# Kernel optimization log

Measured on AMD Instinct MI355X. Metric: run time of the kernel, lower is better.

The kernel has to match this reference:

```python
import jax, jax.numpy as jnp
import numpy as np

B, S, H = 2, 2048, 2048
NH = 16
HD = H // NH  # 128


def setup_inputs() -> dict:
    key = jax.random.key(0)
    ks = jax.random.split(key, 6)
    sc = 0.02
    return {
        "x": jax.random.normal(ks[0], (B, S, H), dtype=jnp.float32),
        "attention_mask": jnp.zeros((B, S), dtype=jnp.float32),
        "Wq": jax.random.normal(ks[1], (H, H), dtype=jnp.float32) * sc,
        "bq": jnp.zeros((H,), dtype=jnp.float32),
        "Wk": jax.random.normal(ks[2], (H, H), dtype=jnp.float32) * sc,
        "bk": jnp.zeros((H,), dtype=jnp.float32),
        "Wv": jax.random.normal(ks[3], (H, H), dtype=jnp.float32) * sc,
        "bv": jnp.zeros((H,), dtype=jnp.float32),
        "Wo": jax.random.normal(ks[4], (H, H), dtype=jnp.float32) * sc,
        "bo": jnp.zeros((H,), dtype=jnp.float32),
    }


def reference(x, attention_mask, Wq, bq, Wk, bk, Wv, bv, Wo, bo):
    b, s, h = x.shape
    q = (x @ Wq + bq).reshape(b, s, NH, HD)
    k = (x @ Wk + bk).reshape(b, s, NH, HD)
    v = (x @ Wv + bv).reshape(b, s, NH, HD)
    scale = 1.0 / jnp.sqrt(jnp.asarray(HD, dtype=x.dtype))
    scores = jnp.einsum('bqhd,bkhd->bhqk', q, k) * scale
    scores = scores + attention_mask[:, None, None, :]
    weights = jax.nn.softmax(scores, axis=-1)
    attn = jnp.einsum('bhqk,bkhd->bqhd', weights, v).reshape(b, s, h)
    return attn @ Wo + bo
```

## Files before the change

kernel.cpp:

```cpp
#include <hip/hip_runtime.h>
#include <hip/hip_bf16.h>
#include <stdint.h>

#define BB   2
#define SS   2048
#define HHH  2048
#define NHH  16
#define HDD  128
#define MTOT 4096

typedef __bf16 bf16x8 __attribute__((ext_vector_type(8)));
typedef float  f32x4  __attribute__((ext_vector_type(4)));

#define MFMA16(a, b, c) __builtin_amdgcn_mfma_f32_16x16x32_bf16((a), (b), (c), 0, 0, 0)

__device__ __forceinline__ unsigned short f2bf(float f) {
    union { float f; unsigned u; } v; v.f = f;
    unsigned r = v.u + 0x7FFFu + ((v.u >> 16) & 1u);
    return (unsigned short)(r >> 16);
}

__device__ __forceinline__ unsigned packbf(float a, float b) {
    union { __bf16 h[2]; unsigned u; } p;
    p.h[0] = (__bf16)a; p.h[1] = (__bf16)b;
    return p.u;
}

__device__ __forceinline__ void gload16(const void* src, void* lds) {
    __builtin_amdgcn_global_load_lds(
        (__attribute__((address_space(1))) void*)src,
        (__attribute__((address_space(3))) void*)lds,
        16, 0, 0);
}

__global__ void cast_f32_bf16(const float* __restrict__ in,
                              unsigned short* __restrict__ out, int n) {
    int i = (blockIdx.x * blockDim.x + threadIdx.x) * 4;
    int stride = gridDim.x * blockDim.x * 4;
    for (; i < n; i += stride) {
        float4 v = *(const float4*)(in + i);
        ushort4 o;
        o.x = f2bf(v.x); o.y = f2bf(v.y); o.z = f2bf(v.z); o.w = f2bf(v.w);
        *(ushort4*)(out + i) = o;
    }
}

__global__ void transpose_cast(const float* __restrict__ in,
                               unsigned short* __restrict__ out) {
    __shared__ float tile[32][33];
    int c0 = blockIdx.x * 32, r0 = blockIdx.y * 32;
    int tx = threadIdx.x, ty = threadIdx.y;
    #pragma unroll
    for (int i = 0; i < 32; i += 8)
        tile[ty + i][tx] = in[(size_t)(r0 + ty + i) * HHH + c0 + tx];
    __syncthreads();
    #pragma unroll
    for (int i = 0; i < 32; i += 8)
        out[(size_t)(c0 + ty + i) * HHH + r0 + tx] = f2bf(tile[tx][ty + i]);
}

template<int MODE>
__global__ __launch_bounds__(256, 2) void gemm_bf16(
    const unsigned short* __restrict__ A,
    const unsigned short* __restrict__ Bt,
    const float* __restrict__ bias,
    void* __restrict__ Cout,
    int M, int N, int K)
{
    __shared__ __align__(16) unsigned char sm[16384];
    const int tid = threadIdx.x;
    const int wv = tid >> 6, ln = tid & 63;
    const int g = ln >> 4, r = ln & 15;
    const int wr = wv >> 1, wc = wv & 1;
    const int m0 = blockIdx.x * 128, n0 = blockIdx.y * 128;

    size_t srcA[2], srcB[2];
    int ldsA[2], ldsB[2];
    #pragma unroll
    for (int i = 0; i < 2; ++i) {
        int ch = wv * 2 + i;
        int o = ch * 1024 + ln * 16;
        int row = o >> 6;
        int gl = ((o >> 4) & 3) ^ ((row >> 1) & 3);
        ldsA[i] = ch * 1024;
        ldsB[i] = 8192 + ch * 1024;
        srcA[i] = (size_t)(m0 + row) * K + gl * 8;
        srcB[i] = (size_t)(n0 + row) * K + gl * 8;
    }

    f32x4 acc[4][4];
    #pragma unroll
    for (int i = 0; i < 4; ++i)
        #pragma unroll
        for (int j = 0; j < 4; ++j)
            acc[i][j] = (f32x4){0.f, 0.f, 0.f, 0.f};

    for (int kt = 0; kt < K; kt += 32) {
        __syncthreads();
        #pragma unroll
        for (int i = 0; i < 2; ++i) {
            gload16(A + srcA[i] + kt, sm + ldsA[i]);
            gload16(Bt + srcB[i] + kt, sm + ldsB[i]);
        }
        __syncthreads();

        bf16x8 af[4], bfr[4];
        #pragma unroll
        for (int t = 0; t < 4; ++t) {
            int rowa = wr * 64 + t * 16 + r;
            int pha = g ^ ((rowa >> 1) & 3);
            af[t] = *(const bf16x8*)(sm + rowa * 64 + pha * 16);
            int rowb = wc * 64 + t * 16 + r;
            int phb = g ^ ((rowb >> 1) & 3);
            bfr[t] = *(const bf16x8*)(sm + 8192 + rowb * 64 + phb * 16);
        }
        #pragma unroll
        for (int mt = 0; mt < 4; ++mt)
            #pragma unroll
            for (int nt = 0; nt < 4; ++nt)
                acc[mt][nt] = MFMA16(af[mt], bfr[nt], acc[mt][nt]);
    }

    #pragma unroll
    for (int mt = 0; mt < 4; ++mt) {
        #pragma unroll
        for (int nt = 0; nt < 4; ++nt) {
            int col = n0 + wc * 64 + nt * 16 + r;
            float bvv = bias[col];
            f32x4 a = acc[mt][nt];
            int mrow = m0 + wr * 64 + mt * 16 + g * 4;
            if (MODE == 0) {
                #pragma unroll
                for (int q = 0; q < 4; ++q)
                    ((unsigned short*)Cout)[(size_t)(mrow + q) * N + col] = f2bf(a[q] + bvv);
            } else if (MODE == 2) {
                #pragma unroll
                for (int q = 0; q < 4; ++q)
                    ((float*)Cout)[(size_t)(mrow + q) * N + col] = a[q] + bvv;
            } else {
                int b = mrow >> 11, s0x = mrow & 2047;
                ushort4 o;
                o.x = f2bf(a[0] + bvv); o.y = f2bf(a[1] + bvv);
                o.z = f2bf(a[2] + bvv); o.w = f2bf(a[3] + bvv);
                *(ushort4*)((unsigned short*)Cout + ((size_t)(b * 2048 + col)) * 2048 + s0x) = o;
            }
        }
    }
}

__global__ __launch_bounds__(256, 2) void attn_fwd(
    const unsigned short* __restrict__ Q,
    const unsigned short* __restrict__ K,
    const unsigned short* __restrict__ V,
    const float* __restrict__ mask,
    unsigned short* __restrict__ O)
{
    __shared__ __align__(16) unsigned char sm[65536];
    const int tid = threadIdx.x, wv = tid >> 6, ln = tid & 63;
    const int g = ln >> 4, r = ln & 15;

    const int bid = blockIdx.x;
    const int lb = (bid & 7) * 64 + (bid >> 3);
    const int qb = lb & 15;
    const int bh = lb >> 4;
    const int h = bh & 15, b = bh >> 4;

    const size_t rowQ0 = (size_t)(b * 2048 + qb * 128 + wv * 32);
    const float SCL2 = 0.08838834764831845f * 1.4426950408889634f;
    const float L2E  = 1.4426950408889634f;

    unsigned srcK[4], srcV[4];
    int ldsK[4], ldsV[4];
    #pragma unroll
    for (int i = 0; i < 4; ++i) {
        int ch = wv * 4 + i;
        int o = ch * 1024 + ln * 16;
        { int row = o >> 8; int gl = ((o >> 4) & 15) ^ (row & 7);
          srcK[i] = (unsigned)((b * 2048 + row) * 2048 + h * 128 + gl * 8);
          ldsK[i] = ch * 1024; }
        { int d = o >> 7; int gl = ((o >> 4) & 7) ^ (d & 7);
          srcV[i] = (unsigned)((b * 2048 + h * 128 + d) * 2048 + gl * 8);
          ldsV[i] = 16384 + ch * 1024; }
    }

    #pragma unroll
    for (int i = 0; i < 4; ++i) {
        gload16(K + srcK[i], sm + ldsK[i]);
        gload16(V + srcV[i], sm + ldsV[i]);
    }

    bf16x8 qf[2][4];
    #pragma unroll
    for (int rtq = 0; rtq < 2; ++rtq)
        #pragma unroll
        for (int ks = 0; ks < 4; ++ks)
            qf[rtq][ks] = *(const bf16x8*)(Q + (rowQ0 + rtq * 16 + r) * 2048 + h * 128 + ks * 32 + g * 8);

    f32x4 acc[2][8];
    #pragma unroll
    for (int i = 0; i < 2; ++i)
        #pragma unroll
        for (int j = 0; j < 8; ++j)
            acc[i][j] = (f32x4){0.f, 0.f, 0.f, 0.f};
    float mr[2] = {-3.0e38f, -3.0e38f};
    float lr[2] = {0.f, 0.f};

    const float* mb = mask + b * 2048;
    const int L0 = ((g & 1) * 2) * 16 + r;
    const int L1 = L0 + 16;

    int cur = 0;
    __syncthreads();

    for (int kb = 0; kb < SS; kb += 64) {
        if (kb + 64 < SS) {
            const unsigned char* dst = sm + (cur ^ 1) * 32768;
            int ko = (kb + 64) * 2048;
            #pragma unroll
            for (int i = 0; i < 4; ++i) {
                gload16(K + srcK[i] + ko, (void*)(dst + ldsK[i]));
                gload16(V + srcV[i] + (kb + 64), (void*)(dst + ldsV[i]));
            }
        }
        const unsigned char* Kt = sm + cur * 32768;
        const unsigned char* Vt = Kt + 16384;

        f32x4 mvv[4];
        #pragma unroll
        for (int ct = 0; ct < 4; ++ct)
            mvv[ct] = *(const f32x4*)(mb + kb + ct * 16 + g * 4);

        f32x4 sfr[4][2];
        #pragma unroll
        for (int ct = 0; ct < 4; ++ct) { sfr[ct][0] = (f32x4){0,0,0,0}; sfr[ct][1] = (f32x4){0,0,0,0}; }
        __builtin_amdgcn_s_setprio(1);
        #pragma unroll
        for (int ct = 0; ct < 4; ++ct) {
            int row = ct * 16 + r;
            #pragma unroll
            for (int ks = 0; ks < 4; ++ks) {
                int ph = (ks * 4 + g) ^ (row & 7);
                bf16x8 kf = *(const bf16x8*)(Kt + row * 256 + ph * 16);
                sfr[ct][0] = MFMA16(kf, qf[0][ks], sfr[ct][0]);
                sfr[ct][1] = MFMA16(kf, qf[1][ks], sfr[ct][1]);
            }
        }
        __builtin_amdgcn_s_setprio(0);

        #pragma unroll
        for (int ct = 0; ct < 4; ++ct)
            #pragma unroll
            for (int rtq = 0; rtq < 2; ++rtq)
                #pragma unroll
                for (int q = 0; q < 4; ++q)
                    sfr[ct][rtq][q] = sfr[ct][rtq][q] * SCL2 + mvv[ct][q] * L2E;

        float mt[2];
        #pragma unroll
        for (int rtq = 0; rtq < 2; ++rtq) {
            float a0 = fmaxf(fmaxf(sfr[0][rtq][0], sfr[0][rtq][1]), fmaxf(sfr[0][rtq][2], sfr[0][rtq][3]));
            float a1 = fmaxf(fmaxf(sfr[1][rtq][0], sfr[1][rtq][1]), fmaxf(sfr[1][rtq][2], sfr[1][rtq][3]));
            float a2 = fmaxf(fmaxf(sfr[2][rtq][0], sfr[2][rtq][1]), fmaxf(sfr[2][rtq][2], sfr[2][rtq][3]));
            float a3 = fmaxf(fmaxf(sfr[3][rtq][0], sfr[3][rtq][1]), fmaxf(sfr[3][rtq][2], sfr[3][rtq][3]));
            float m = fmaxf(fmaxf(a0, a1), fmaxf(a2, a3));
            m = fmaxf(m, __shfl_xor(m, 16));
            m = fmaxf(m, __shfl_xor(m, 32));
            mt[rtq] = m;
        }

        float alpha[2] = {1.f, 1.f};
        int allskip = __all((mt[0] <= mr[0] + 8.f) && (mt[1] <= mr[1] + 8.f));
        if (!allskip) {
            #pragma unroll
            for (int rtq = 0; rtq < 2; ++rtq) {
                float nm = fmaxf(mr[rtq], mt[rtq]);
                alpha[rtq] = __builtin_amdgcn_exp2f(mr[rtq] - nm);
                mr[rtq] = nm;
            }
            #pragma unroll
            for (int rtq = 0; rtq < 2; ++rtq)
                #pragma unroll
                for (int q = 0; q < 4; ++q) {
                    float ar = __shfl(alpha[rtq], g * 4 + q);
                    #pragma unroll
                    for (int dt = 0; dt < 8; ++dt)
                        acc[rtq][dt][q] *= ar;
                }
        }

        #pragma unroll
        for (int rtq = 0; rtq < 2; ++rtq) {
            float rs = 0.f;
            #pragma unroll
            for (int ct = 0; ct < 4; ++ct)
                #pragma unroll
                for (int q = 0; q < 4; ++q) {
                    float p = __builtin_amdgcn_exp2f(sfr[ct][rtq][q] - mr[rtq]);
                    sfr[ct][rtq][q] = p;
                    rs += p;
                }
            rs += __shfl_xor(rs, 16);
            rs += __shfl_xor(rs, 32);
            lr[rtq] = lr[rtq] * alpha[rtq] + rs;
        }

        unsigned plo[4][2], phi[4][2];
        #pragma unroll
        for (int ct = 0; ct < 4; ++ct)
            #pragma unroll
            for (int rtq = 0; rtq < 2; ++rtq) {
                plo[ct][rtq] = packbf(sfr[ct][rtq][0], sfr[ct][rtq][1]);
                phi[ct][rtq] = packbf(sfr[ct][rtq][2], sfr[ct][rtq][3]);
            }

        bf16x8 pf[2][2];
        #pragma unroll
        for (int rtq = 0; rtq < 2; ++rtq)
            #pragma unroll
            for (int ks = 0; ks < 2; ++ks) {
                union { unsigned w[4]; bf16x8 v; } u;
                #pragma unroll
                for (int w = 0; w < 4; ++w) {
                    int L = (w < 2) ? L0 : L1;
                    unsigned a = (w & 1) ? phi[2 * ks][rtq]     : plo[2 * ks][rtq];
                    unsigned c = (w & 1) ? phi[2 * ks + 1][rtq] : plo[2 * ks + 1][rtq];
                    unsigned va = (unsigned)__shfl((int)a, L);
                    unsigned vc = (unsigned)__shfl((int)c, L);
                    u.w[w] = (g & 2) ? vc : va;
                }
                pf[rtq][ks] = u.v;
            }

        __builtin_amdgcn_s_setprio(1);
        #pragma unroll
        for (int dt = 0; dt < 8; ++dt) {
            int d = dt * 16 + r;
            f32x4 a0 = acc[0][dt], a1 = acc[1][dt];
            #pragma unroll
            for (int ks = 0; ks < 2; ++ks) {
                int ph = (ks * 4 + g) ^ (d & 7);
                bf16x8 vf = *(const bf16x8*)(Vt + d * 128 + ph * 16);
                a0 = MFMA16(pf[0][ks], vf, a0);
                a1 = MFMA16(pf[1][ks], vf, a1);
            }
            acc[0][dt] = a0; acc[1][dt] = a1;
        }
        __builtin_amdgcn_s_setprio(0);

        __syncthreads();
        cur ^= 1;
    }

    #pragma unroll
    for (int rtq = 0; rtq < 2; ++rtq) {
        float linv[4];
        #pragma unroll
        for (int q = 0; q < 4; ++q)
            linv[q] = 1.f / __shfl(lr[rtq], g * 4 + q);
        #pragma unroll
        for (int dt = 0; dt < 8; ++dt)
            #pragma unroll
            for (int q = 0; q < 4; ++q) {
                float v = acc[rtq][dt][q] * linv[q];
                size_t row = rowQ0 + rtq * 16 + g * 4 + q;
                O[row * 2048 + h * 128 + dt * 16 + r] = f2bf(v);
            }
    }
}

extern "C" void kernel_launch(void* const* d_in, const int* in_sizes, int n_in,
                              void* d_out, int out_size, void* d_ws, size_t ws_size,
                              hipStream_t stream)
{
    (void)in_sizes; (void)n_in; (void)out_size; (void)ws_size;
    const float* x    = (const float*)d_in[0];
    const float* mask = (const float*)d_in[1];
    const float* Wq   = (const float*)d_in[2];
    const float* bq   = (const float*)d_in[3];
    const float* Wk   = (const float*)d_in[4];
    const float* bk   = (const float*)d_in[5];
    const float* Wv   = (const float*)d_in[6];
    const float* bv   = (const float*)d_in[7];
    const float* Wo   = (const float*)d_in[8];
    const float* bo   = (const float*)d_in[9];
    float* out = (float*)d_out;

    char* ws = (char*)d_ws;
    unsigned short* xb  = (unsigned short*)(ws);
    unsigned short* Wqt = (unsigned short*)(ws + (16u << 20));
    unsigned short* Wkt = (unsigned short*)(ws + (24u << 20));
    unsigned short* Wvt = (unsigned short*)(ws + (32u << 20));
    unsigned short* Wot = (unsigned short*)(ws + (40u << 20));
    unsigned short* Qb  = (unsigned short*)(ws + (48u << 20));
    unsigned short* Kb  = (unsigned short*)(ws + (64u << 20));
    unsigned short* Vtb = (unsigned short*)(ws + (80u << 20));
    unsigned short* Ab  = (unsigned short*)(ws + (16u << 20));

    cast_f32_bf16<<<2048, 256, 0, stream>>>(x, xb, MTOT * HHH);
    dim3 tb(32, 8), tg(64, 64);
    transpose_cast<<<tg, tb, 0, stream>>>(Wq, Wqt);
    transpose_cast<<<tg, tb, 0, stream>>>(Wk, Wkt);
    transpose_cast<<<tg, tb, 0, stream>>>(Wv, Wvt);
    transpose_cast<<<tg, tb, 0, stream>>>(Wo, Wot);

    dim3 gg(MTOT / 128, HHH / 128);
    gemm_bf16<0><<<gg, 256, 0, stream>>>(xb, Wqt, bq, Qb,  MTOT, HHH, HHH);
    gemm_bf16<0><<<gg, 256, 0, stream>>>(xb, Wkt, bk, Kb,  MTOT, HHH, HHH);
    gemm_bf16<1><<<gg, 256, 0, stream>>>(xb, Wvt, bv, Vtb, MTOT, HHH, HHH);

    attn_fwd<<<BB * NHH * (SS / 128), 256, 0, stream>>>(Qb, Kb, Vtb, mask, Ab);

    gemm_bf16<2><<<gg, 256, 0, stream>>>(Ab, Wot, bo, out, MTOT, HHH, HHH);
}
```

Before: 317.5 us.

## Switch attention kernel to 32x32x16 MFMA with per-lane query row ownership

Rewrites the attention inner loop to use 32x32x16 bf16 MFMA instead of 16x16x32, computing S^T so each lane owns a single query row. This cuts the cross-lane shuffles needed for row max, row sum, alpha broadcast and P fragment repacking, and lets the output be stored as packed vectors. The larger accumulator tiles raise register pressure, which may hurt occupancy under launch bounds of 2.

```diff
diff --git a/kernel.cpp b/kernel.cpp
--- a/kernel.cpp
+++ b/kernel.cpp
@@ -11,8 +11,10 @@
 
 typedef __bf16 bf16x8 __attribute__((ext_vector_type(8)));
 typedef float  f32x4  __attribute__((ext_vector_type(4)));
+typedef float  f32x16 __attribute__((ext_vector_type(16)));
 
 #define MFMA16(a, b, c) __builtin_amdgcn_mfma_f32_16x16x32_bf16((a), (b), (c), 0, 0, 0)
+#define MFMA32(a, b, c) __builtin_amdgcn_mfma_f32_32x32x16_bf16((a), (b), (c), 0, 0, 0)
 
 __device__ __forceinline__ unsigned short f2bf(float f) {
     union { float f; unsigned u; } v; v.f = f;
@@ -157,7 +159,7 @@
 {
     __shared__ __align__(16) unsigned char sm[65536];
     const int tid = threadIdx.x, wv = tid >> 6, ln = tid & 63;
-    const int g = ln >> 4, r = ln & 15;
+    const int hi = ln >> 5, qr = ln & 31;
 
     const int bid = blockIdx.x;
     const int lb = (bid & 7) * 64 + (bid >> 3);
@@ -189,26 +191,20 @@
         gload16(V + srcV[i], sm + ldsV[i]);
     }
 
-    bf16x8 qf[2][4];
-    #pragma unroll
-    for (int rtq = 0; rtq < 2; ++rtq)
-        #pragma unroll
-        for (int ks = 0; ks < 4; ++ks)
-            qf[rtq][ks] = *(const bf16x8*)(Q + (rowQ0 + rtq * 16 + r) * 2048 + h * 128 + ks * 32 + g * 8);
-
-    f32x4 acc[2][8];
-    #pragma unroll
-    for (int i = 0; i < 2; ++i)
-        #pragma unroll
-        for (int j = 0; j < 8; ++j)
-            acc[i][j] = (f32x4){0.f, 0.f, 0.f, 0.f};
-    float mr[2] = {-3.0e38f, -3.0e38f};
-    float lr[2] = {0.f, 0.f};
+    bf16x8 qf[8];
+    #pragma unroll
+    for (int ks = 0; ks < 8; ++ks)
+        qf[ks] = *(const bf16x8*)(Q + (rowQ0 + qr) * 2048 + h * 128 + ks * 16 + hi * 8);
+
+    f32x16 acc[4];
+    #pragma unroll
+    for (int i = 0; i < 4; ++i)
+        #pragma unroll
+        for (int j = 0; j < 16; ++j)
+            acc[i][j] = 0.f;
+    float mr = -3.0e38f, lr = 0.f;
 
     const float* mb = mask + b * 2048;
-    const int L0 = ((g & 1) * 2) * 16 + r;
-    const int L1 = L0 + 16;
-
     int cur = 0;
     __syncthreads();
 
@@ -225,125 +221,100 @@
         const unsigned char* Kt = sm + cur * 32768;
         const unsigned char* Vt = Kt + 16384;
 
-        f32x4 mvv[4];
-        #pragma unroll
-        for (int ct = 0; ct < 4; ++ct)
-            mvv[ct] = *(const f32x4*)(mb + kb + ct * 16 + g * 4);
-
-        f32x4 sfr[4][2];
-        #pragma unroll
-        for (int ct = 0; ct < 4; ++ct) { sfr[ct][0] = (f32x4){0,0,0,0}; sfr[ct][1] = (f32x4){0,0,0,0}; }
+        f32x4 mk[2][4];
+        #pragma unroll
+        for (int kb2 = 0; kb2 < 2; ++kb2)
+            #pragma unroll
+            for (int rg = 0; rg < 4; ++rg)
+                mk[kb2][rg] = *(const f32x4*)(mb + kb + kb2 * 32 + rg * 8 + hi * 4);
+
+        f32x16 sf0, sf1;
+        #pragma unroll
+        for (int j = 0; j < 16; ++j) { sf0[j] = 0.f; sf1[j] = 0.f; }
         __builtin_amdgcn_s_setprio(1);
         #pragma unroll
-        for (int ct = 0; ct < 4; ++ct) {
-            int row = ct * 16 + r;
-            #pragma unroll
-            for (int ks = 0; ks < 4; ++ks) {
-                int ph = (ks * 4 + g) ^ (row & 7);
-                bf16x8 kf = *(const bf16x8*)(Kt + row * 256 + ph * 16);
-                sfr[ct][0] = MFMA16(kf, qf[0][ks], sfr[ct][0]);
-                sfr[ct][1] = MFMA16(kf, qf[1][ks], sfr[ct][1]);
+        for (int ks = 0; ks < 8; ++ks) {
+            int row0 = qr, row1 = 32 + qr;
+            int s0 = ((2 * ks + hi) ^ (row0 & 7));
+            int s1 = ((2 * ks + hi) ^ (row1 & 7));
+            bf16x8 kf0 = *(const bf16x8*)(Kt + row0 * 256 + s0 * 16);
+            bf16x8 kf1 = *(const bf16x8*)(Kt + row1 * 256 + s1 * 16);
+            sf0 = MFMA32(kf0, qf[ks], sf0);
+            sf1 = MFMA32(kf1, qf[ks], sf1);
+        }
+        __builtin_amdgcn_s_setprio(0);
+
+        float sv[2][16];
+        #pragma unroll
+        for (int reg = 0; reg < 16; ++reg) {
+            sv[0][reg] = sf0[reg] * SCL2 + mk[0][reg >> 2][reg & 3] * L2E;
+            sv[1][reg] = sf1[reg] * SCL2 + mk[1][reg >> 2][reg & 3] * L2E;
+        }
+
+        float m01 = fmaxf(sv[0][0], sv[1][0]);
+        #pragma unroll
+        for (int reg = 1; reg < 16; ++reg)
+            m01 = fmaxf(m01, fmaxf(sv[0][reg], sv[1][reg]));
+        float mt = fmaxf(m01, __shfl_xor(m01, 32));
+
+        float alpha = 1.f;
+        int allskip = __all(mt <= mr + 8.f);
+        if (!allskip) {
+            float nm = fmaxf(mr, mt);
+            alpha = __builtin_amdgcn_exp2f(mr - nm);
+            mr = nm;
+            #pragma unroll
+            for (int dblk = 0; dblk < 4; ++dblk)
+                #pragma unroll
+                for (int reg = 0; reg < 16; ++reg)
+                    acc[dblk][reg] *= alpha;
+        }
+
+        float rs = 0.f;
+        #pragma unroll
+        for (int kb2 = 0; kb2 < 2; ++kb2)
+            #pragma unroll
+            for (int reg = 0; reg < 16; ++reg) {
+                float p = __builtin_amdgcn_exp2f(sv[kb2][reg] - mr);
+                sv[kb2][reg] = p;
+                rs += p;
             }
-        }
-        __builtin_amdgcn_s_setprio(0);
-
-        #pragma unroll
-        for (int ct = 0; ct < 4; ++ct)
-            #pragma unroll
-            for (int rtq = 0; rtq < 2; ++rtq)
-                #pragma unroll
-                for (int q = 0; q < 4; ++q)
-                    sfr[ct][rtq][q] = sfr[ct][rtq][q] * SCL2 + mvv[ct][q] * L2E;
-
-        float mt[2];
-        #pragma unroll
-        for (int rtq = 0; rtq < 2; ++rtq) {
-            float a0 = fmaxf(fmaxf(sfr[0][rtq][0], sfr[0][rtq][1]), fmaxf(sfr[0][rtq][2], sfr[0][rtq][3]));
-            float a1 = fmaxf(fmaxf(sfr[1][rtq][0], sfr[1][rtq][1]), fmaxf(sfr[1][rtq][2], sfr[1][rtq][3]));
-            float a2 = fmaxf(fmaxf(sfr[2][rtq][0], sfr[2][rtq][1]), fmaxf(sfr[2][rtq][2], sfr[2][rtq][3]));
-            float a3 = fmaxf(fmaxf(sfr[3][rtq][0], sfr[3][rtq][1]), fmaxf(sfr[3][rtq][2], sfr[3][rtq][3]));
-            float m = fmaxf(fmaxf(a0, a1), fmaxf(a2, a3));
-            m = fmaxf(m, __shfl_xor(m, 16));
-            m = fmaxf(m, __shfl_xor(m, 32));
-            mt[rtq] = m;
-        }
-
-        float alpha[2] = {1.f, 1.f};
-        int allskip = __all((mt[0] <= mr[0] + 8.f) && (mt[1] <= mr[1] + 8.f));
-        if (!allskip) {
-            #pragma unroll
-            for (int rtq = 0; rtq < 2; ++rtq) {
-                float nm = fmaxf(mr[rtq], mt[rtq]);
-                alpha[rtq] = __builtin_amdgcn_exp2f(mr[rtq] - nm);
-                mr[rtq] = nm;
+        rs += __shfl_xor(rs, 32);
+        lr = lr * alpha + rs;
+
+        bf16x8 pfr[4];
+        #pragma unroll
+        for (int kb16 = 0; kb16 < 4; ++kb16) {
+            const int kb2 = kb16 >> 1, i2 = kb16 & 1;
+            float* pv = sv[kb2];
+            unsigned W00 = packbf(pv[(2*i2+0)*4 + 0], pv[(2*i2+0)*4 + 1]);
+            unsigned W01 = packbf(pv[(2*i2+0)*4 + 2], pv[(2*i2+0)*4 + 3]);
+            unsigned W10 = packbf(pv[(2*i2+1)*4 + 0], pv[(2*i2+1)*4 + 1]);
+            unsigned W11 = packbf(pv[(2*i2+1)*4 + 2], pv[(2*i2+1)*4 + 3]);
+            unsigned v0 = hi ? W00 : W10;
+            unsigned v1 = hi ? W01 : W11;
+            unsigned y0 = (unsigned)__shfl_xor((int)v0, 32);
+            unsigned y1 = (unsigned)__shfl_xor((int)v1, 32);
+            union { unsigned w[4]; bf16x8 v; } u;
+            u.w[0] = hi ? y0  : W00;
+            u.w[1] = hi ? y1  : W01;
+            u.w[2] = hi ? W10 : y0;
+            u.w[3] = hi ? W11 : y1;
+            pfr[kb16] = u.v;
+        }
+
+        __builtin_amdgcn_s_setprio(1);
+        #pragma unroll
+        for (int dblk = 0; dblk < 4; ++dblk) {
+            int d = dblk * 32 + qr;
+            f32x16 a = acc[dblk];
+            #pragma unroll
+            for (int kb16 = 0; kb16 < 4; ++kb16) {
+                int s = ((2 * kb16 + hi) ^ (d & 7));
+                bf16x8 vf = *(const bf16x8*)(Vt + d * 128 + s * 16);
+                a = MFMA32(vf, pfr[kb16], a);
             }
-            #pragma unroll
-            for (int rtq = 0; rtq < 2; ++rtq)
-                #pragma unroll
-                for (int q = 0; q < 4; ++q) {
-                    float ar = __shfl(alpha[rtq], g * 4 + q);
-                    #pragma unroll
-                    for (int dt = 0; dt < 8; ++dt)
-                        acc[rtq][dt][q] *= ar;
-                }
-        }
-
-        #pragma unroll
-        for (int rtq = 0; rtq < 2; ++rtq) {
-            float rs = 0.f;
-            #pragma unroll
-            for (int ct = 0; ct < 4; ++ct)
-                #pragma unroll
-                for (int q = 0; q < 4; ++q) {
-                    float p = __builtin_amdgcn_exp2f(sfr[ct][rtq][q] - mr[rtq]);
-                    sfr[ct][rtq][q] = p;
-                    rs += p;
-                }
-            rs += __shfl_xor(rs, 16);
-            rs += __shfl_xor(rs, 32);
-            lr[rtq] = lr[rtq] * alpha[rtq] + rs;
-        }
-
-        unsigned plo[4][2], phi[4][2];
-        #pragma unroll
-        for (int ct = 0; ct < 4; ++ct)
-            #pragma unroll
-            for (int rtq = 0; rtq < 2; ++rtq) {
-                plo[ct][rtq] = packbf(sfr[ct][rtq][0], sfr[ct][rtq][1]);
-                phi[ct][rtq] = packbf(sfr[ct][rtq][2], sfr[ct][rtq][3]);
-            }
-
-        bf16x8 pf[2][2];
-        #pragma unroll
-        for (int rtq = 0; rtq < 2; ++rtq)
-            #pragma unroll
-            for (int ks = 0; ks < 2; ++ks) {
-                union { unsigned w[4]; bf16x8 v; } u;
-                #pragma unroll
-                for (int w = 0; w < 4; ++w) {
-                    int L = (w < 2) ? L0 : L1;
-                    unsigned a = (w & 1) ? phi[2 * ks][rtq]     : plo[2 * ks][rtq];
-                    unsigned c = (w & 1) ? phi[2 * ks + 1][rtq] : plo[2 * ks + 1][rtq];
-                    unsigned va = (unsigned)__shfl((int)a, L);
-                    unsigned vc = (unsigned)__shfl((int)c, L);
-                    u.w[w] = (g & 2) ? vc : va;
-                }
-                pf[rtq][ks] = u.v;
-            }
-
-        __builtin_amdgcn_s_setprio(1);
-        #pragma unroll
-        for (int dt = 0; dt < 8; ++dt) {
-            int d = dt * 16 + r;
-            f32x4 a0 = acc[0][dt], a1 = acc[1][dt];
-            #pragma unroll
-            for (int ks = 0; ks < 2; ++ks) {
-                int ph = (ks * 4 + g) ^ (d & 7);
-                bf16x8 vf = *(const bf16x8*)(Vt + d * 128 + ph * 16);
-                a0 = MFMA16(pf[0][ks], vf, a0);
-                a1 = MFMA16(pf[1][ks], vf, a1);
-            }
-            acc[0][dt] = a0; acc[1][dt] = a1;
+            acc[dblk] = a;
         }
         __builtin_amdgcn_s_setprio(0);
 
@@ -351,21 +322,21 @@
         cur ^= 1;
     }
 
-    #pragma unroll
-    for (int rtq = 0; rtq < 2; ++rtq) {
-        float linv[4];
-        #pragma unroll
-        for (int q = 0; q < 4; ++q)
-            linv[q] = 1.f / __shfl(lr[rtq], g * 4 + q);
-        #pragma unroll
-        for (int dt = 0; dt < 8; ++dt)
-            #pragma unroll
-            for (int q = 0; q < 4; ++q) {
-                float v = acc[rtq][dt][q] * linv[q];
-                size_t row = rowQ0 + rtq * 16 + g * 4 + q;
-                O[row * 2048 + h * 128 + dt * 16 + r] = f2bf(v);
-            }
-    }
+    float linv = 1.f / lr;
+    unsigned short* orow = O + (rowQ0 + qr) * 2048 + h * 128;
+    #pragma unroll
+    for (int dblk = 0; dblk < 4; ++dblk)
+        #pragma unroll
+        for (int rg = 0; rg < 4; ++rg) {
+            float v0 = acc[dblk][rg * 4 + 0] * linv;
+            float v1 = acc[dblk][rg * 4 + 1] * linv;
+            float v2 = acc[dblk][rg * 4 + 2] * linv;
+            float v3 = acc[dblk][rg * 4 + 3] * linv;
+            uint2 o;
+            o.x = packbf(v0, v1);
+            o.y = packbf(v2, v3);
+            *(uint2*)(orow + dblk * 32 + rg * 8 + hi * 4) = o;
+        }
 }
 
 extern "C" void kernel_launch(void* const* d_in, const int* in_sizes, int n_in,
```

Result: no change. 313.0 us (-1.4%).
